# Optimization experiments

Measured on AMD Instinct MI355X. Metric: run time of the kernel, lower is better.

The kernel has to match this reference:

```python
import jax, jax.numpy as jnp
import numpy as np

N_NODES = 50000
N_EDGES = 800000


def gcn_conv(x, edge_index, W, b):
    """PyG GCNConv: add self-loops, symmetric deg^{-1/2} normalization,
    dense transform, scatter-add aggregation."""
    n = x.shape[0]
    src, dst = edge_index[0], edge_index[1]
    # add self-loops
    loop = jnp.arange(n, dtype=src.dtype)
    src = jnp.concatenate([src, loop])
    dst = jnp.concatenate([dst, loop])
    # degree on destination nodes (includes self-loops -> deg >= 1)
    deg = jax.ops.segment_sum(jnp.ones_like(dst, dtype=x.dtype), dst, num_segments=n)
    dinv = jax.lax.rsqrt(deg)
    norm = dinv[src] * dinv[dst]  # [E+N]
    h = x @ W                     # [N, F_out] dense GEMM
    msg = h[src] * norm[:, None]  # gather + scale, [E+N, F_out]
    out = jax.ops.segment_sum(msg, dst, num_segments=n)  # scatter-add
    return out + b


def setup_inputs() -> dict:
    key = jax.random.key(0)
    ks = jax.random.split(key, 8)
    x = jax.random.normal(ks[0], (N_NODES, 100), dtype=jnp.float32)
    edge_index = jax.random.randint(ks[1], (2, N_EDGES), 0, N_NODES, dtype=jnp.int64)
    W1 = jax.random.normal(ks[2], (100, 256), dtype=jnp.float32) * 0.1
    b1 = jnp.zeros((256,), dtype=jnp.float32)
    W2 = jax.random.normal(ks[3], (256, 128), dtype=jnp.float32) * 0.06
    b2 = jnp.zeros((128,), dtype=jnp.float32)
    Wfc = jax.random.normal(ks[4], (128, 1), dtype=jnp.float32) * 0.09
    bfc = jnp.zeros((1,), dtype=jnp.float32)
    return {"x": x, "edge_index": edge_index, "W1": W1, "b1": b1,
            "W2": W2, "b2": b2, "Wfc": Wfc, "bfc": bfc}


def reference(x, edge_index, W1, b1, W2, b2, Wfc, bfc):
    # eval mode: F.dropout with training=False is identity
    h = jax.nn.relu(gcn_conv(x, edge_index, W1, b1))
    h = jax.nn.relu(gcn_conv(h, edge_index, W2, b2))
    return h @ Wfc + bfc  # [N, 1]
```

## Files before the change

kernel.cpp:

```cpp
#include <hip/hip_runtime.h>
#include <hip/hip_bf16.h>


#define F0 100
#define F1 256
#define F2 128


__global__ void zero_i32(int* p, int n) {
    int i = blockIdx.x * blockDim.x + threadIdx.x;
    if (i < n) p[i] = 0;
}

__global__ void deg_count_i(const int* __restrict__ dst, int* deg, int e) {
    int i = blockIdx.x * blockDim.x + threadIdx.x;
    if (i < e) atomicAdd(deg + dst[i], 1);
}

__global__ __launch_bounds__(256) void scan1(const int* __restrict__ deg,
                                             int* __restrict__ excl,
                                             int* __restrict__ bsum,
                                             float* __restrict__ dinv, int n) {
    __shared__ int wsum[4];
    int i = blockIdx.x * 256 + threadIdx.x;
    int lane = threadIdx.x & 63, wid = threadIdx.x >> 6;
    int v = (i < n) ? deg[i] : 0;
    if (i < n) dinv[i] = rsqrtf((float)(v + 1));
    int s = v;
#pragma unroll
    for (int off = 1; off < 64; off <<= 1) {
        int t = __shfl_up(s, off, 64);
        if (lane >= off) s += t;
    }
    if (lane == 63) wsum[wid] = s;
    __syncthreads();
    int add = 0;
    for (int w = 0; w < wid; w++) add += wsum[w];
    if (i < n) excl[i] = add + s - v;
    if (threadIdx.x == 255) bsum[blockIdx.x] = add + s;
}

__global__ __launch_bounds__(256) void scan2(int* __restrict__ bsum, int nb,
                                             int* __restrict__ rowptr, int n) {
    __shared__ int wsum[4];
    int lane = threadIdx.x & 63, wid = threadIdx.x >> 6;
    int v = (threadIdx.x < nb) ? bsum[threadIdx.x] : 0;
    int s = v;
#pragma unroll
    for (int off = 1; off < 64; off <<= 1) {
        int t = __shfl_up(s, off, 64);
        if (lane >= off) s += t;
    }
    if (lane == 63) wsum[wid] = s;
    __syncthreads();
    int add = 0;
    for (int w = 0; w < wid; w++) add += wsum[w];
    if (threadIdx.x < nb) bsum[threadIdx.x] = add + s - v;
    if (threadIdx.x == 255) rowptr[n] = add + s;
}

__global__ void scan3(const int* __restrict__ excl, const int* __restrict__ bsum,
                      int* __restrict__ rowptr, int* __restrict__ cursor, int n) {
    int i = blockIdx.x * 256 + threadIdx.x;
    if (i < n) {
        int r = excl[i] + bsum[blockIdx.x];
        rowptr[i] = r;
        cursor[i] = r;
    }
}

__global__ void csr_fill(const int* __restrict__ src, const int* __restrict__ dst,
                         int* cursor, int* __restrict__ csr, int e) {
    int i = blockIdx.x * blockDim.x + threadIdx.x;
    if (i < e) {
        int pos = atomicAdd(cursor + dst[i], 1);
        csr[pos] = src[i];
    }
}


__global__ __launch_bounds__(256) void pull_f100(
        const float* __restrict__ x, const int* __restrict__ rowptr,
        const int* __restrict__ csr, const float* __restrict__ dinv,
        float* __restrict__ agg, int n) {
    int wave = threadIdx.x >> 6, lane = threadIdx.x & 63;
    int v = blockIdx.x * 4 + wave;
    if (v >= n) return;
    int beg = rowptr[v], end = rowptr[v + 1];
    float dv = dinv[v];
    int half = lane >> 5;
    int q = lane & 31;
    bool act = q < 25;
    float4 acc = {0.f, 0.f, 0.f, 0.f};

    for (int base = beg; base < end; base += 64) {
        int cnt = min(64, end - base);
        int sidx = (lane < cnt) ? csr[base + lane] : v;
        float scoef = (lane < cnt) ? dinv[sidx] : 0.f;
        int npairs = (cnt + 1) >> 1;
        int p = 0;
        for (; p + 4 <= npairs; p += 4) {
            int s0 = __shfl(sidx, 2 * p + half, 64);
            int s1 = __shfl(sidx, 2 * (p + 1) + half, 64);
            int s2 = __shfl(sidx, 2 * (p + 2) + half, 64);
            int s3 = __shfl(sidx, 2 * (p + 3) + half, 64);
            float c0 = __shfl(scoef, 2 * p + half, 64);
            float c1 = __shfl(scoef, 2 * (p + 1) + half, 64);
            float c2 = __shfl(scoef, 2 * (p + 2) + half, 64);
            float c3 = __shfl(scoef, 2 * (p + 3) + half, 64);
            if (act) {
                float4 r0 = ((const float4*)(x + (size_t)s0 * F0))[q];
                float4 r1 = ((const float4*)(x + (size_t)s1 * F0))[q];
                float4 r2 = ((const float4*)(x + (size_t)s2 * F0))[q];
                float4 r3 = ((const float4*)(x + (size_t)s3 * F0))[q];
                acc.x += c0 * r0.x + c1 * r1.x + c2 * r2.x + c3 * r3.x;
                acc.y += c0 * r0.y + c1 * r1.y + c2 * r2.y + c3 * r3.y;
                acc.z += c0 * r0.z + c1 * r1.z + c2 * r2.z + c3 * r3.z;
                acc.w += c0 * r0.w + c1 * r1.w + c2 * r2.w + c3 * r3.w;
            }
        }
        for (; p < npairs; p++) {
            int s0 = __shfl(sidx, 2 * p + half, 64);
            float c0 = __shfl(scoef, 2 * p + half, 64);
            if (act) {
                float4 r0 = ((const float4*)(x + (size_t)s0 * F0))[q];
                acc.x += c0 * r0.x;
                acc.y += c0 * r0.y;
                acc.z += c0 * r0.z;
                acc.w += c0 * r0.w;
            }
        }
    }
    float ox = __shfl_down(acc.x, 32, 64);
    float oy = __shfl_down(acc.y, 32, 64);
    float oz = __shfl_down(acc.z, 32, 64);
    float ow = __shfl_down(acc.w, 32, 64);
    if (half == 0 && act) {
        float4 hv = ((const float4*)(x + (size_t)v * F0))[q];
        float4 r;
        r.x = dv * (acc.x + ox + dv * hv.x);
        r.y = dv * (acc.y + oy + dv * hv.y);
        r.z = dv * (acc.z + oz + dv * hv.z);
        r.w = dv * (acc.w + ow + dv * hv.w);
        ((float4*)(agg + (size_t)v * F0))[q] = r;
    }
}

__global__ __launch_bounds__(256) void pull_f128_fused(
        const float* __restrict__ h2, const int* __restrict__ rowptr,
        const int* __restrict__ csr, const float* __restrict__ dinv,
        const float* __restrict__ b2, const float* __restrict__ Wfc,
        const float* __restrict__ bfc, float* __restrict__ out, int n) {
    int wave = threadIdx.x >> 6, lane = threadIdx.x & 63;
    int v = blockIdx.x * 4 + wave;
    if (v >= n) return;
    int beg = rowptr[v], end = rowptr[v + 1];
    float dv = dinv[v];
    int half = lane >> 5;
    int q = lane & 31;
    float4 acc = {0.f, 0.f, 0.f, 0.f};

    for (int base = beg; base < end; base += 64) {
        int cnt = min(64, end - base);
        int sidx = (lane < cnt) ? csr[base + lane] : v;
        float scoef = (lane < cnt) ? dinv[sidx] : 0.f;
        int npairs = (cnt + 1) >> 1;
        int p = 0;
        for (; p + 4 <= npairs; p += 4) {
            int s0 = __shfl(sidx, 2 * p + half, 64);
            int s1 = __shfl(sidx, 2 * (p + 1) + half, 64);
            int s2 = __shfl(sidx, 2 * (p + 2) + half, 64);
            int s3 = __shfl(sidx, 2 * (p + 3) + half, 64);
            float c0 = __shfl(scoef, 2 * p + half, 64);
            float c1 = __shfl(scoef, 2 * (p + 1) + half, 64);
            float c2 = __shfl(scoef, 2 * (p + 2) + half, 64);
            float c3 = __shfl(scoef, 2 * (p + 3) + half, 64);
            float4 r0 = ((const float4*)(h2 + (size_t)s0 * F2))[q];
            float4 r1 = ((const float4*)(h2 + (size_t)s1 * F2))[q];
            float4 r2 = ((const float4*)(h2 + (size_t)s2 * F2))[q];
            float4 r3 = ((const float4*)(h2 + (size_t)s3 * F2))[q];
            acc.x += c0 * r0.x + c1 * r1.x + c2 * r2.x + c3 * r3.x;
            acc.y += c0 * r0.y + c1 * r1.y + c2 * r2.y + c3 * r3.y;
            acc.z += c0 * r0.z + c1 * r1.z + c2 * r2.z + c3 * r3.z;
            acc.w += c0 * r0.w + c1 * r1.w + c2 * r2.w + c3 * r3.w;
        }
        for (; p < npairs; p++) {
            int s0 = __shfl(sidx, 2 * p + half, 64);
            float c0 = __shfl(scoef, 2 * p + half, 64);
            float4 r0 = ((const float4*)(h2 + (size_t)s0 * F2))[q];
            acc.x += c0 * r0.x;
            acc.y += c0 * r0.y;
            acc.z += c0 * r0.z;
            acc.w += c0 * r0.w;
        }
    }
    float ox = __shfl_down(acc.x, 32, 64);
    float oy = __shfl_down(acc.y, 32, 64);
    float oz = __shfl_down(acc.z, 32, 64);
    float ow = __shfl_down(acc.w, 32, 64);
    float part = 0.f;
    if (half == 0) {
        float4 hv = ((const float4*)(h2 + (size_t)v * F2))[q];
        float4 b2v = ((const float4*)b2)[q];
        float4 wv = ((const float4*)Wfc)[q];
        float t0 = dv * (acc.x + ox + dv * hv.x);
        float t1 = dv * (acc.y + oy + dv * hv.y);
        float t2 = dv * (acc.z + oz + dv * hv.z);
        float t3 = dv * (acc.w + ow + dv * hv.w);
        part = fmaxf(t0 + b2v.x, 0.f) * wv.x + fmaxf(t1 + b2v.y, 0.f) * wv.y +
               fmaxf(t2 + b2v.z, 0.f) * wv.z + fmaxf(t3 + b2v.w, 0.f) * wv.w;
        part += __shfl_down(part, 16, 64);
        part += __shfl_down(part, 8, 64);
        part += __shfl_down(part, 4, 64);
        part += __shfl_down(part, 2, 64);
        part += __shfl_down(part, 1, 64);
        if (lane == 0) out[v] = part + bfc[0];
    }
}


__global__ __launch_bounds__(256) void gemm1_tiled(
        const float* __restrict__ A, const float* __restrict__ W,
        const float* __restrict__ bias, float* __restrict__ C, int n) {
    __shared__ float As[20 * 128];
    __shared__ float Bs[20 * 128];
    int tid = threadIdx.x;
    int r0 = blockIdx.x * 128;
    int c0 = blockIdx.y * 128;
    int tc = tid & 15, tr = tid >> 4;
    float acc[8][8] = {};

    for (int k0 = 0; k0 < F0; k0 += 20) {
        if (k0) __syncthreads();
        for (int idx = tid; idx < 128 * 5; idx += 256) {
            int row = idx & 127, kq = idx >> 7;
            int gr = r0 + row;
            if (gr >= n) gr = n - 1;
            float4 v = *(const float4*)(A + (size_t)gr * F0 + k0 + 4 * kq);
            As[(4 * kq + 0) * 128 + row] = v.x;
            As[(4 * kq + 1) * 128 + row] = v.y;
            As[(4 * kq + 2) * 128 + row] = v.z;
            As[(4 * kq + 3) * 128 + row] = v.w;
        }
        for (int idx = tid; idx < 20 * 32; idx += 256) {
            int k = idx >> 5, cq = idx & 31;
            *(float4*)(Bs + k * 128 + 4 * cq) =
                *(const float4*)(W + (size_t)(k0 + k) * F1 + c0 + 4 * cq);
        }
        __syncthreads();
#pragma unroll 5
        for (int k = 0; k < 20; k++) {
            float4 a0 = *(const float4*)(As + k * 128 + 4 * tr);
            float4 a1 = *(const float4*)(As + k * 128 + 64 + 4 * tr);
            float4 b0 = *(const float4*)(Bs + k * 128 + 4 * tc);
            float4 b1 = *(const float4*)(Bs + k * 128 + 64 + 4 * tc);
            float av[8] = {a0.x, a0.y, a0.z, a0.w, a1.x, a1.y, a1.z, a1.w};
            float bv[8] = {b0.x, b0.y, b0.z, b0.w, b1.x, b1.y, b1.z, b1.w};
#pragma unroll
            for (int i = 0; i < 8; i++)
#pragma unroll
                for (int j = 0; j < 8; j++) acc[i][j] += av[i] * bv[j];
        }
    }
    float4 bb0 = *(const float4*)(bias + c0 + 4 * tc);
    float4 bb1 = *(const float4*)(bias + c0 + 64 + 4 * tc);
    float bv[8] = {bb0.x, bb0.y, bb0.z, bb0.w, bb1.x, bb1.y, bb1.z, bb1.w};
#pragma unroll
    for (int i = 0; i < 8; i++) {
        int row = (i < 4) ? (4 * tr + i) : (64 + 4 * tr + i - 4);
        int gr = r0 + row;
        if (gr < n) {
            float4 o0, o1;
            o0.x = fmaxf(acc[i][0] + bv[0], 0.f);
            o0.y = fmaxf(acc[i][1] + bv[1], 0.f);
            o0.z = fmaxf(acc[i][2] + bv[2], 0.f);
            o0.w = fmaxf(acc[i][3] + bv[3], 0.f);
            o1.x = fmaxf(acc[i][4] + bv[4], 0.f);
            o1.y = fmaxf(acc[i][5] + bv[5], 0.f);
            o1.z = fmaxf(acc[i][6] + bv[6], 0.f);
            o1.w = fmaxf(acc[i][7] + bv[7], 0.f);
            *(float4*)(C + (size_t)gr * F1 + c0 + 4 * tc) = o0;
            *(float4*)(C + (size_t)gr * F1 + c0 + 64 + 4 * tc) = o1;
        }
    }
}

__global__ __launch_bounds__(256) void gemm2_tiled(
        const float* __restrict__ A, const float* __restrict__ W,
        float* __restrict__ C, int n) {
    __shared__ float As[32 * 128];
    __shared__ float Bs[32 * 128];
    int tid = threadIdx.x;
    int r0 = blockIdx.x * 128;
    int tc = tid & 15, tr = tid >> 4;
    float acc[8][8] = {};

    for (int k0 = 0; k0 < F1; k0 += 32) {
        if (k0) __syncthreads();
        for (int idx = tid; idx < 128 * 8; idx += 256) {
            int row = idx & 127, kq = idx >> 7;
            int gr = r0 + row;
            if (gr >= n) gr = n - 1;
            float4 v = *(const float4*)(A + (size_t)gr * F1 + k0 + 4 * kq);
            As[(4 * kq + 0) * 128 + row] = v.x;
            As[(4 * kq + 1) * 128 + row] = v.y;
            As[(4 * kq + 2) * 128 + row] = v.z;
            As[(4 * kq + 3) * 128 + row] = v.w;
        }
        for (int idx = tid; idx < 32 * 32; idx += 256) {
            int k = idx >> 5, cq = idx & 31;
            *(float4*)(Bs + k * 128 + 4 * cq) =
                *(const float4*)(W + (size_t)(k0 + k) * F2 + 4 * cq);
        }
        __syncthreads();
#pragma unroll 4
        for (int k = 0; k < 32; k++) {
            float4 a0 = *(const float4*)(As + k * 128 + 4 * tr);
            float4 a1 = *(const float4*)(As + k * 128 + 64 + 4 * tr);
            float4 b0 = *(const float4*)(Bs + k * 128 + 4 * tc);
            float4 b1 = *(const float4*)(Bs + k * 128 + 64 + 4 * tc);
            float av[8] = {a0.x, a0.y, a0.z, a0.w, a1.x, a1.y, a1.z, a1.w};
            float bv[8] = {b0.x, b0.y, b0.z, b0.w, b1.x, b1.y, b1.z, b1.w};
#pragma unroll
            for (int i = 0; i < 8; i++)
#pragma unroll
                for (int j = 0; j < 8; j++) acc[i][j] += av[i] * bv[j];
        }
    }
#pragma unroll
    for (int i = 0; i < 8; i++) {
        int row = (i < 4) ? (4 * tr + i) : (64 + 4 * tr + i - 4);
        int gr = r0 + row;
        if (gr < n) {
            float4 o0 = {acc[i][0], acc[i][1], acc[i][2], acc[i][3]};
            float4 o1 = {acc[i][4], acc[i][5], acc[i][6], acc[i][7]};
            *(float4*)(C + (size_t)gr * F2 + 4 * tc) = o0;
            *(float4*)(C + (size_t)gr * F2 + 64 + 4 * tc) = o1;
        }
    }
}


static inline size_t align16(size_t x) { return (x + 3) & ~(size_t)3; }

extern "C" void kernel_launch(void* const* d_in, const int* in_sizes, int n_in,
                              void* d_out, int out_size, void* d_ws, size_t ws_size,
                              hipStream_t stream) {
    const float* x   = (const float*)d_in[0];
    const int*   ei  = (const int*)d_in[1];
    const float* W1  = (const float*)d_in[2];
    const float* b1  = (const float*)d_in[3];
    const float* W2  = (const float*)d_in[4];
    const float* b2  = (const float*)d_in[5];
    const float* Wfc = (const float*)d_in[6];
    const float* bfc = (const float*)d_in[7];
    float* out = (float*)d_out;

    const int n = in_sizes[0] / F0;
    const int e = in_sizes[1] / 2;
    const int* src = ei;
    const int* dst = ei + e;

    char* wsb = (char*)d_ws;
    size_t off = 0;
    int* deg    = (int*)(wsb + 4 * off); off = align16(off + n);
    int* excl   = (int*)(wsb + 4 * off); off = align16(off + n);
    int* bsum   = (int*)(wsb + 4 * off); off = align16(off + 256);
    int* rowptr = (int*)(wsb + 4 * off); off = align16(off + n + 1);
    int* cursor = (int*)(wsb + 4 * off); off = align16(off + n);
    int* csr    = (int*)(wsb + 4 * off); off = align16(off + e);
    float* dinv = (float*)(wsb + 4 * off); off = align16(off + n);
    float* aggX = (float*)(wsb + 4 * off); off = align16(off + (size_t)n * F0);
    float* a1   = (float*)(wsb + 4 * off); off = align16(off + (size_t)n * F1);
    float* h2   = (float*)(wsb + 4 * off); off = align16(off + (size_t)n * F2);

    const int B = 256;
    const int nb = (n + B - 1) / B;
    const int rblocks = (n + 127) / 128;

    zero_i32<<<nb, B, 0, stream>>>(deg, n);
    deg_count_i<<<(e + B - 1) / B, B, 0, stream>>>(dst, deg, e);
    scan1<<<nb, B, 0, stream>>>(deg, excl, bsum, dinv, n);
    scan2<<<1, B, 0, stream>>>(bsum, nb, rowptr, n);
    scan3<<<nb, B, 0, stream>>>(excl, bsum, rowptr, cursor, n);
    csr_fill<<<(e + B - 1) / B, B, 0, stream>>>(src, dst, cursor, csr, e);

    pull_f100<<<(n + 3) / 4, 256, 0, stream>>>(x, rowptr, csr, dinv, aggX, n);
    gemm1_tiled<<<dim3(rblocks, F1 / 128), 256, 0, stream>>>(aggX, W1, b1, a1, n);

    gemm2_tiled<<<rblocks, 256, 0, stream>>>(a1, W2, h2, n);
    pull_f128_fused<<<(n + 3) / 4, 256, 0, stream>>>(h2, rowptr, csr, dinv,
                                                     b2, Wfc, bfc, out, n);
}
```

Before: 387.5 us.

## Prescale features by dinv to drop per-edge coefficients, and register-prefetch GEMM tiles

Source-node features are multiplied by deg^{-1/2} once, in a new scale_x kernel for layer 1 and in the gemm2 epilogue for layer 2. The pull kernels then only sum neighbor rows, which removes the per-edge dinv gather, the coefficient shuffles and the multiplies, and the self-loop term is folded into the accumulator init. Both tiled GEMMs now prefetch the next K-chunk from global memory into registers while the current shared-memory tile is being computed. In exchange the change adds an extra N×100 pass plus its buffer, and extra syncs and register pressure in the GEMMs.

Result: slower. 415.6 us (+7.2%).

```diff
diff --git a/kernel.cpp b/kernel.cpp
--- a/kernel.cpp
+++ b/kernel.cpp
@@ -78,9 +78,21 @@
     }
 }
 
+__global__ void scale_x(const float4* __restrict__ x4,
+                        const float* __restrict__ dinv,
+                        float4* __restrict__ xs4, int n25) {
+    int i = blockIdx.x * blockDim.x + threadIdx.x;
+    if (i < n25) {
+        float d = dinv[i / 25];
+        float4 v = x4[i];
+        v.x *= d; v.y *= d; v.z *= d; v.w *= d;
+        xs4[i] = v;
+    }
+}
+
 
 __global__ __launch_bounds__(256) void pull_f100(
-        const float* __restrict__ x, const int* __restrict__ rowptr,
+        const float* __restrict__ xs, const int* __restrict__ rowptr,
         const int* __restrict__ csr, const float* __restrict__ dinv,
         float* __restrict__ agg, int n) {
     int wave = threadIdx.x >> 6, lane = threadIdx.x & 63;
@@ -88,46 +100,44 @@
     if (v >= n) return;
     int beg = rowptr[v], end = rowptr[v + 1];
     float dv = dinv[v];
-    int half = lane >> 5;
-    int q = lane & 31;
+    int half = lane >> 5, q = lane & 31;
     bool act = q < 25;
     float4 acc = {0.f, 0.f, 0.f, 0.f};
+    if (half == 0 && act) acc = ((const float4*)(xs + (size_t)v * F0))[q];
 
     for (int base = beg; base < end; base += 64) {
         int cnt = min(64, end - base);
-        int sidx = (lane < cnt) ? csr[base + lane] : v;
-        float scoef = (lane < cnt) ? dinv[sidx] : 0.f;
-        int npairs = (cnt + 1) >> 1;
+        int sidx = (lane < cnt) ? csr[base + lane] : 0;
+        int npf = cnt >> 1;
         int p = 0;
-        for (; p + 4 <= npairs; p += 4) {
+        for (; p + 4 <= npf; p += 4) {
             int s0 = __shfl(sidx, 2 * p + half, 64);
-            int s1 = __shfl(sidx, 2 * (p + 1) + half, 64);
-            int s2 = __shfl(sidx, 2 * (p + 2) + half, 64);
-            int s3 = __shfl(sidx, 2 * (p + 3) + half, 64);
-            float c0 = __shfl(scoef, 2 * p + half, 64);
-            float c1 = __shfl(scoef, 2 * (p + 1) + half, 64);
-            float c2 = __shfl(scoef, 2 * (p + 2) + half, 64);
-            float c3 = __shfl(scoef, 2 * (p + 3) + half, 64);
+            int s1 = __shfl(sidx, 2 * p + 2 + half, 64);
+            int s2 = __shfl(sidx, 2 * p + 4 + half, 64);
+            int s3 = __shfl(sidx, 2 * p + 6 + half, 64);
             if (act) {
-                float4 r0 = ((const float4*)(x + (size_t)s0 * F0))[q];
-                float4 r1 = ((const float4*)(x + (size_t)s1 * F0))[q];
-                float4 r2 = ((const float4*)(x + (size_t)s2 * F0))[q];
-                float4 r3 = ((const float4*)(x + (size_t)s3 * F0))[q];
-                acc.x += c0 * r0.x + c1 * r1.x + c2 * r2.x + c3 * r3.x;
-                acc.y += c0 * r0.y + c1 * r1.y + c2 * r2.y + c3 * r3.y;
-                acc.z += c0 * r0.z + c1 * r1.z + c2 * r2.z + c3 * r3.z;
-                acc.w += c0 * r0.w + c1 * r1.w + c2 * r2.w + c3 * r3.w;
-            }
-        }
-        for (; p < npairs; p++) {
+                float4 r0 = ((const float4*)(xs + (size_t)s0 * F0))[q];
+                float4 r1 = ((const float4*)(xs + (size_t)s1 * F0))[q];
+                float4 r2 = ((const float4*)(xs + (size_t)s2 * F0))[q];
+                float4 r3 = ((const float4*)(xs + (size_t)s3 * F0))[q];
+                acc.x += (r0.x + r1.x) + (r2.x + r3.x);
+                acc.y += (r0.y + r1.y) + (r2.y + r3.y);
+                acc.z += (r0.z + r1.z) + (r2.z + r3.z);
+                acc.w += (r0.w + r1.w) + (r2.w + r3.w);
+            }
+        }
+        for (; p < npf; p++) {
             int s0 = __shfl(sidx, 2 * p + half, 64);
-            float c0 = __shfl(scoef, 2 * p + half, 64);
             if (act) {
-                float4 r0 = ((const float4*)(x + (size_t)s0 * F0))[q];
-                acc.x += c0 * r0.x;
-                acc.y += c0 * r0.y;
-                acc.z += c0 * r0.z;
-                acc.w += c0 * r0.w;
+                float4 r0 = ((const float4*)(xs + (size_t)s0 * F0))[q];
+                acc.x += r0.x; acc.y += r0.y; acc.z += r0.z; acc.w += r0.w;
+            }
+        }
+        if (cnt & 1) {
+            int sl = __shfl(sidx, cnt - 1, 64);
+            if (half == 0 && act) {
+                float4 r = ((const float4*)(xs + (size_t)sl * F0))[q];
+                acc.x += r.x; acc.y += r.y; acc.z += r.z; acc.w += r.w;
             }
         }
     }
@@ -136,18 +146,17 @@
     float oz = __shfl_down(acc.z, 32, 64);
     float ow = __shfl_down(acc.w, 32, 64);
     if (half == 0 && act) {
-        float4 hv = ((const float4*)(x + (size_t)v * F0))[q];
         float4 r;
-        r.x = dv * (acc.x + ox + dv * hv.x);
-        r.y = dv * (acc.y + oy + dv * hv.y);
-        r.z = dv * (acc.z + oz + dv * hv.z);
-        r.w = dv * (acc.w + ow + dv * hv.w);
+        r.x = dv * (acc.x + ox);
+        r.y = dv * (acc.y + oy);
+        r.z = dv * (acc.z + oz);
+        r.w = dv * (acc.w + ow);
         ((float4*)(agg + (size_t)v * F0))[q] = r;
     }
 }
 
 __global__ __launch_bounds__(256) void pull_f128_fused(
-        const float* __restrict__ h2, const int* __restrict__ rowptr,
+        const float* __restrict__ h2s, const int* __restrict__ rowptr,
         const int* __restrict__ csr, const float* __restrict__ dinv,
         const float* __restrict__ b2, const float* __restrict__ Wfc,
         const float* __restrict__ bfc, float* __restrict__ out, int n) {
@@ -156,59 +165,55 @@
     if (v >= n) return;
     int beg = rowptr[v], end = rowptr[v + 1];
     float dv = dinv[v];
-    int half = lane >> 5;
-    int q = lane & 31;
+    int half = lane >> 5, q = lane & 31;
     float4 acc = {0.f, 0.f, 0.f, 0.f};
+    if (half == 0) acc = ((const float4*)(h2s + (size_t)v * F2))[q];
 
     for (int base = beg; base < end; base += 64) {
         int cnt = min(64, end - base);
-        int sidx = (lane < cnt) ? csr[base + lane] : v;
-        float scoef = (lane < cnt) ? dinv[sidx] : 0.f;
-        int npairs = (cnt + 1) >> 1;
+        int sidx = (lane < cnt) ? csr[base + lane] : 0;
+        int npf = cnt >> 1;
         int p = 0;
-        for (; p + 4 <= npairs; p += 4) {
+        for (; p + 4 <= npf; p += 4) {
             int s0 = __shfl(sidx, 2 * p + half, 64);
-            int s1 = __shfl(sidx, 2 * (p + 1) + half, 64);
-            int s2 = __shfl(sidx, 2 * (p + 2) + half, 64);
-            int s3 = __shfl(sidx, 2 * (p + 3) + half, 64);
-            float c0 = __shfl(scoef, 2 * p + half, 64);
-            float c1 = __shfl(scoef, 2 * (p + 1) + half, 64);
-            float c2 = __shfl(scoef, 2 * (p + 2) + half, 64);
-            float c3 = __shfl(scoef, 2 * (p + 3) + half, 64);
-            float4 r0 = ((const float4*)(h2 + (size_t)s0 * F2))[q];
-            float4 r1 = ((const float4*)(h2 + (size_t)s1 * F2))[q];
-            float4 r2 = ((const float4*)(h2 + (size_t)s2 * F2))[q];
-            float4 r3 = ((const float4*)(h2 + (size_t)s3 * F2))[q];
-            acc.x += c0 * r0.x + c1 * r1.x + c2 * r2.x + c3 * r3.x;
-            acc.y += c0 * r0.y + c1 * r1.y + c2 * r2.y + c3 * r3.y;
-            acc.z += c0 * r0.z + c1 * r1.z + c2 * r2.z + c3 * r3.z;
-            acc.w += c0 * r0.w + c1 * r1.w + c2 * r2.w + c3 * r3.w;
-        }
-        for (; p < npairs; p++) {
+            int s1 = __shfl(sidx, 2 * p + 2 + half, 64);
+            int s2 = __shfl(sidx, 2 * p + 4 + half, 64);
+            int s3 = __shfl(sidx, 2 * p + 6 + half, 64);
+            float4 r0 = ((const float4*)(h2s + (size_t)s0 * F2))[q];
+            float4 r1 = ((const float4*)(h2s + (size_t)s1 * F2))[q];
+            float4 r2 = ((const float4*)(h2s + (size_t)s2 * F2))[q];
+            float4 r3 = ((const float4*)(h2s + (size_t)s3 * F2))[q];
+            acc.x += (r0.x + r1.x) + (r2.x + r3.x);
+            acc.y += (r0.y + r1.y) + (r2.y + r3.y);
+            acc.z += (r0.z + r1.z) + (r2.z + r3.z);
+            acc.w += (r0.w + r1.w) + (r2.w + r3.w);
+        }
+        for (; p < npf; p++) {
             int s0 = __shfl(sidx, 2 * p + half, 64);
-            float c0 = __shfl(scoef, 2 * p + half, 64);
-            float4 r0 = ((const float4*)(h2 + (size_t)s0 * F2))[q];
-            acc.x += c0 * r0.x;
-            acc.y += c0 * r0.y;
-            acc.z += c0 * r0.z;
-            acc.w += c0 * r0.w;
+            float4 r0 = ((const float4*)(h2s + (size_t)s0 * F2))[q];
+            acc.x += r0.x; acc.y += r0.y; acc.z += r0.z; acc.w += r0.w;
+        }
+        if (cnt & 1) {
+            int sl = __shfl(sidx, cnt - 1, 64);
+            if (half == 0) {
+                float4 r = ((const float4*)(h2s + (size_t)sl * F2))[q];
+                acc.x += r.x; acc.y += r.y; acc.z += r.z; acc.w += r.w;
+            }
         }
     }
     float ox = __shfl_down(acc.x, 32, 64);
     float oy = __shfl_down(acc.y, 32, 64);
     float oz = __shfl_down(acc.z, 32, 64);
     float ow = __shfl_down(acc.w, 32, 64);
-    float part = 0.f;
     if (half == 0) {
-        float4 hv = ((const float4*)(h2 + (size_t)v * F2))[q];
         float4 b2v = ((const float4*)b2)[q];
         float4 wv = ((const float4*)Wfc)[q];
-        float t0 = dv * (acc.x + ox + dv * hv.x);
-        float t1 = dv * (acc.y + oy + dv * hv.y);
-        float t2 = dv * (acc.z + oz + dv * hv.z);
-        float t3 = dv * (acc.w + ow + dv * hv.w);
-        part = fmaxf(t0 + b2v.x, 0.f) * wv.x + fmaxf(t1 + b2v.y, 0.f) * wv.y +
-               fmaxf(t2 + b2v.z, 0.f) * wv.z + fmaxf(t3 + b2v.w, 0.f) * wv.w;
+        float t0 = dv * (acc.x + ox);
+        float t1 = dv * (acc.y + oy);
+        float t2 = dv * (acc.z + oz);
+        float t3 = dv * (acc.w + ow);
+        float part = fmaxf(t0 + b2v.x, 0.f) * wv.x + fmaxf(t1 + b2v.y, 0.f) * wv.y +
+                     fmaxf(t2 + b2v.z, 0.f) * wv.z + fmaxf(t3 + b2v.w, 0.f) * wv.w;
         part += __shfl_down(part, 16, 64);
         part += __shfl_down(part, 8, 64);
         part += __shfl_down(part, 4, 64);
@@ -225,29 +230,47 @@
     __shared__ float As[20 * 128];
     __shared__ float Bs[20 * 128];
     int tid = threadIdx.x;
-    int r0 = blockIdx.x * 128;
-    int c0 = blockIdx.y * 128;
+    int r0 = blockIdx.x * 128, c0 = blockIdx.y * 128;
     int tc = tid & 15, tr = tid >> 4;
     float acc[8][8] = {};
-
-    for (int k0 = 0; k0 < F0; k0 += 20) {
-        if (k0) __syncthreads();
-        for (int idx = tid; idx < 128 * 5; idx += 256) {
-            int row = idx & 127, kq = idx >> 7;
-            int gr = r0 + row;
-            if (gr >= n) gr = n - 1;
-            float4 v = *(const float4*)(A + (size_t)gr * F0 + k0 + 4 * kq);
-            As[(4 * kq + 0) * 128 + row] = v.x;
-            As[(4 * kq + 1) * 128 + row] = v.y;
-            As[(4 * kq + 2) * 128 + row] = v.z;
-            As[(4 * kq + 3) * 128 + row] = v.w;
-        }
-        for (int idx = tid; idx < 20 * 32; idx += 256) {
-            int k = idx >> 5, cq = idx & 31;
-            *(float4*)(Bs + k * 128 + 4 * cq) =
-                *(const float4*)(W + (size_t)(k0 + k) * F1 + c0 + 4 * cq);
-        }
+    float4 pa[3], pb[3];
+    const int NL = 640;
+
+    auto ld = [&](int k0) {
+#pragma unroll
+        for (int j = 0; j < 3; j++) {
+            int idx = tid + 256 * j;
+            if (idx < NL) {
+                int row = idx & 127, kq = idx >> 7;
+                int gr = r0 + row;
+                if (gr >= n) gr = n - 1;
+                pa[j] = *(const float4*)(A + (size_t)gr * F0 + k0 + 4 * kq);
+                int k = idx >> 5, cq = idx & 31;
+                pb[j] = *(const float4*)(W + (size_t)(k0 + k) * F1 + c0 + 4 * cq);
+            }
+        }
+    };
+    auto st = [&]() {
+#pragma unroll
+        for (int j = 0; j < 3; j++) {
+            int idx = tid + 256 * j;
+            if (idx < NL) {
+                int row = idx & 127, kq = idx >> 7;
+                As[(4 * kq + 0) * 128 + row] = pa[j].x;
+                As[(4 * kq + 1) * 128 + row] = pa[j].y;
+                As[(4 * kq + 2) * 128 + row] = pa[j].z;
+                As[(4 * kq + 3) * 128 + row] = pa[j].w;
+                int k = idx >> 5, cq = idx & 31;
+                *(float4*)(Bs + k * 128 + 4 * cq) = pb[j];
+            }
+        }
+    };
+
+    ld(0);
+    for (int c = 0; c < 5; c++) {
+        st();
         __syncthreads();
+        if (c < 4) ld(20 * (c + 1));
 #pragma unroll 5
         for (int k = 0; k < 20; k++) {
             float4 a0 = *(const float4*)(As + k * 128 + 4 * tr);
@@ -261,6 +284,7 @@
 #pragma unroll
                 for (int j = 0; j < 8; j++) acc[i][j] += av[i] * bv[j];
         }
+        __syncthreads();
     }
     float4 bb0 = *(const float4*)(bias + c0 + 4 * tc);
     float4 bb1 = *(const float4*)(bias + c0 + 64 + 4 * tc);
@@ -287,32 +311,46 @@
 
 __global__ __launch_bounds__(256) void gemm2_tiled(
         const float* __restrict__ A, const float* __restrict__ W,
-        float* __restrict__ C, int n) {
+        const float* __restrict__ dinv, float* __restrict__ C, int n) {
     __shared__ float As[32 * 128];
     __shared__ float Bs[32 * 128];
     int tid = threadIdx.x;
     int r0 = blockIdx.x * 128;
     int tc = tid & 15, tr = tid >> 4;
     float acc[8][8] = {};
-
-    for (int k0 = 0; k0 < F1; k0 += 32) {
-        if (k0) __syncthreads();
-        for (int idx = tid; idx < 128 * 8; idx += 256) {
+    float4 pa[4], pb[4];
+
+    auto ld = [&](int k0) {
+#pragma unroll
+        for (int j = 0; j < 4; j++) {
+            int idx = tid + 256 * j;
             int row = idx & 127, kq = idx >> 7;
             int gr = r0 + row;
             if (gr >= n) gr = n - 1;
-            float4 v = *(const float4*)(A + (size_t)gr * F1 + k0 + 4 * kq);
-            As[(4 * kq + 0) * 128 + row] = v.x;
-            As[(4 * kq + 1) * 128 + row] = v.y;
-            As[(4 * kq + 2) * 128 + row] = v.z;
-            As[(4 * kq + 3) * 128 + row] = v.w;
-        }
-        for (int idx = tid; idx < 32 * 32; idx += 256) {
+            pa[j] = *(const float4*)(A + (size_t)gr * F1 + k0 + 4 * kq);
             int k = idx >> 5, cq = idx & 31;
-            *(float4*)(Bs + k * 128 + 4 * cq) =
-                *(const float4*)(W + (size_t)(k0 + k) * F2 + 4 * cq);
-        }
+            pb[j] = *(const float4*)(W + (size_t)(k0 + k) * F2 + 4 * cq);
+        }
+    };
+    auto st = [&]() {
+#pragma unroll
+        for (int j = 0; j < 4; j++) {
+            int idx = tid + 256 * j;
+            int row = idx & 127, kq = idx >> 7;
+            As[(4 * kq + 0) * 128 + row] = pa[j].x;
+            As[(4 * kq + 1) * 128 + row] = pa[j].y;
+            As[(4 * kq + 2) * 128 + row] = pa[j].z;
+            As[(4 * kq + 3) * 128 + row] = pa[j].w;
+            int k = idx >> 5, cq = idx & 31;
+            *(float4*)(Bs + k * 128 + 4 * cq) = pb[j];
+        }
+    };
+
+    ld(0);
+    for (int c = 0; c < 8; c++) {
+        st();
         __syncthreads();
+        if (c < 7) ld(32 * (c + 1));
 #pragma unroll 4
         for (int k = 0; k < 32; k++) {
             float4 a0 = *(const float4*)(As + k * 128 + 4 * tr);
@@ -326,14 +364,16 @@
 #pragma unroll
                 for (int j = 0; j < 8; j++) acc[i][j] += av[i] * bv[j];
         }
+        __syncthreads();
     }
 #pragma unroll
     for (int i = 0; i < 8; i++) {
         int row = (i < 4) ? (4 * tr + i) : (64 + 4 * tr + i - 4);
         int gr = r0 + row;
         if (gr < n) {
-            float4 o0 = {acc[i][0], acc[i][1], acc[i][2], acc[i][3]};
-            float4 o1 = {acc[i][4], acc[i][5], acc[i][6], acc[i][7]};
+            float d = dinv[gr];
+            float4 o0 = {acc[i][0] * d, acc[i][1] * d, acc[i][2] * d, acc[i][3] * d};
+            float4 o1 = {acc[i][4] * d, acc[i][5] * d, acc[i][6] * d, acc[i][7] * d};
             *(float4*)(C + (size_t)gr * F2 + 4 * tc) = o0;
             *(float4*)(C + (size_t)gr * F2 + 64 + 4 * tc) = o1;
         }
@@ -370,9 +410,10 @@
     int* cursor = (int*)(wsb + 4 * off); off = align16(off + n);
     int* csr    = (int*)(wsb + 4 * off); off = align16(off + e);
     float* dinv = (float*)(wsb + 4 * off); off = align16(off + n);
+    float* xs   = (float*)(wsb + 4 * off); off = align16(off + (size_t)n * F0);
     float* aggX = (float*)(wsb + 4 * off); off = align16(off + (size_t)n * F0);
     float* a1   = (float*)(wsb + 4 * off); off = align16(off + (size_t)n * F1);
-    float* h2   = (float*)(wsb + 4 * off); off = align16(off + (size_t)n * F2);
+    float* h2s  = (float*)(wsb + 4 * off); off = align16(off + (size_t)n * F2);
 
     const int B = 256;
     const int nb = (n + B - 1) / B;
@@ -381,14 +422,16 @@
     zero_i32<<<nb, B, 0, stream>>>(deg, n);
     deg_count_i<<<(e + B - 1) / B, B, 0, stream>>>(dst, deg, e);
     scan1<<<nb, B, 0, stream>>>(deg, excl, bsum, dinv, n);
+    scale_x<<<((n * 25) + B - 1) / B, B, 0, stream>>>(
+        (const float4*)x, dinv, (float4*)xs, n * 25);
     scan2<<<1, B, 0, stream>>>(bsum, nb, rowptr, n);
     scan3<<<nb, B, 0, stream>>>(excl, bsum, rowptr, cursor, n);
     csr_fill<<<(e + B - 1) / B, B, 0, stream>>>(src, dst, cursor, csr, e);
 
-    pull_f100<<<(n + 3) / 4, 256, 0, stream>>>(x, rowptr, csr, dinv, aggX, n);
+    pull_f100<<<(n + 3) / 4, 256, 0, stream>>>(xs, rowptr, csr, dinv, aggX, n);
     gemm1_tiled<<<dim3(rblocks, F1 / 128), 256, 0, stream>>>(aggX, W1, b1, a1, n);
 
-    gemm2_tiled<<<rblocks, 256, 0, stream>>>(a1, W2, h2, n);
-    pull_f128_fused<<<(n + 3) / 4, 256, 0, stream>>>(h2, rowptr, csr, dinv,
+    gemm2_tiled<<<rblocks, 256, 0, stream>>>(a1, W2, dinv, h2s, n);
+    pull_f128_fused<<<(n + 3) / 4, 256, 0, stream>>>(h2s, rowptr, csr, dinv,
                                                      b2, Wfc, bfc, out, n);
 }
```
